# Kernel tuning notes

Measured on AMD Instinct MI355X. Metric: run time of the kernel, lower is better.

Reference implementation:

```python
import jax, jax.numpy as jnp
import numpy as np

N, E, T, D = 50000, 800000, 400000, 64


def _linear_params(key, fan_in, fan_out):
    kw, kb = jax.random.split(key)
    s = 1.0 / np.sqrt(fan_in)
    W = jax.random.uniform(kw, (fan_in, fan_out), minval=-s, maxval=s, dtype=jnp.float32)
    b = jax.random.uniform(kb, (fan_out,), minval=-s, maxval=s, dtype=jnp.float32)
    return W, b


def setup_inputs() -> dict:
    key = jax.random.key(0)
    ks = jax.random.split(key, 11)
    Ws1, bs1 = _linear_params(ks[0], 2 * D, D)
    Ws2, bs2 = _linear_params(ks[1], D, 3 * D)
    Wc1, bc1 = _linear_params(ks[2], 2 * D, D)
    Wc2, bc2 = _linear_params(ks[3], D, D)
    WV, bV = _linear_params(ks[4], D, D)
    return {
        "node_scalar": jax.random.normal(ks[5], (N, D), dtype=jnp.float32),
        "node_chiral": jax.random.normal(ks[6], (N, D), dtype=jnp.float32),
        "node_vector": jax.random.normal(ks[7], (N, 3, D), dtype=jnp.float32),
        "pos": jax.random.normal(ks[8], (N, 3), dtype=jnp.float32),
        "edge_index": jax.random.randint(ks[9], (E, 2), 0, N, dtype=jnp.int64),
        "triplet_index": jax.random.randint(ks[10], (T, 4), 0, N, dtype=jnp.int64),
        "Ws1": Ws1, "bs1": bs1, "Ws2": Ws2, "bs2": bs2,
        "Wc1": Wc1, "bc1": bc1, "Wc2": Wc2, "bc2": bc2,
        "WV": WV, "bV": bV,
    }


def reference(node_scalar, node_chiral, node_vector, pos, edge_index, triplet_index,
              Ws1, bs1, Ws2, bs2, Wc1, bc1, Wc2, bc2, WV, bV):
    n = node_scalar.shape[0]
    d = node_scalar.shape[1]
    e0, e1 = edge_index[:, 0], edge_index[:, 1]

    # Scalar / vector section: gather -> Linear-SiLU-Linear gate -> scatter-add
    g = jax.nn.silu(jnp.concatenate([node_scalar[e0], node_scalar[e1]], axis=1) @ Ws1 + bs1) @ Ws2 + bs2
    gate_vector, gate_edge, messages_ss = jnp.split(g, 3, axis=1)  # each [E, d]
    messages_vv = gate_vector[:, None, :] * node_vector[e1]               # [E, 3, d]
    rel = pos[e1] - pos[e0]                                               # [E, 3]
    messages_ev = gate_edge[:, None, :] * rel[:, :, None]                 # [E, 3, d]
    msg_ss = jax.ops.segment_sum(messages_ss, e0, num_segments=n)
    msg_vv = jax.ops.segment_sum(messages_vv, e0, num_segments=n)
    msg_ev = jax.ops.segment_sum(messages_ev, e0, num_segments=n)

    Vv = node_vector @ WV + bV          # [N, 3, d]
    Vv_norm = jnp.linalg.norm(Vv, axis=1)  # [N, d] (norm over spatial axis)
    message_vs = node_scalar * Vv_norm

    # Chiral section: triplet gathers, shared gate MLP, scalar triple product
    base, t1, t2, t3 = (triplet_index[:, i] for i in range(4))
    hc_base = node_chiral[base]

    def cgate(other):
        h = jnp.concatenate([hc_base, node_chiral[other]], axis=1)
        return jax.nn.silu(h @ Wc1 + bc1) @ Wc2 + bc2

    chiral_gate = cgate(t1) + cgate(t2) + cgate(t3)  # [T, d]
    pb = pos[base]
    r1, r2, r3 = pb - pos[t1], pb - pos[t2], pb - pos[t3]
    stp = jnp.einsum('ei,ei->e', r1, jnp.cross(r2, r3))  # scalar triple product [T]
    chiral_messages = chiral_gate / (stp + 0.01)[:, None]
    msg_chiral = jax.ops.segment_sum(chiral_messages, base, num_segments=n)

    return (node_scalar + msg_ss + message_vs,
            node_chiral + msg_chiral,
            node_vector + msg_vv + msg_ev)
```

## Files before the change

kernel.cpp:

```cpp
#include <hip/hip_runtime.h>
#include <math.h>

#define DD 64
typedef unsigned short ushort_t;
typedef __attribute__((ext_vector_type(8))) short bf16x8;
typedef __attribute__((ext_vector_type(4))) float f32x4;

__device__ __forceinline__ float silu_f(float x) {
    return x / (1.0f + __expf(-x));
}

__device__ __forceinline__ unsigned f32_to_bf16_rne(float x) {
    unsigned u = __float_as_uint(x);
    unsigned r = ((u >> 16) & 1u) + 0x7fffu;
    return (u + r) >> 16;
}

__device__ __forceinline__ float bf16_to_f32(ushort_t v) {
    return __uint_as_float(((unsigned)v) << 16);
}

__device__ __forceinline__ void gload_lds4(const void* gsrc, void* lds_base) {
    __builtin_amdgcn_global_load_lds(
        (const __attribute__((address_space(1))) void*)gsrc,
        (__attribute__((address_space(3))) void*)lds_base,
        4, 0, 0);
}

#define RFL(x) __builtin_amdgcn_readfirstlane(x)

__global__ __launch_bounds__(256) void rel_kernel(const int* __restrict__ eidx,
                                                  const float* __restrict__ pos,
                                                  float* __restrict__ relg, int E)
{
    int e = blockIdx.x * 256 + threadIdx.x;
    if (e < E) {
        int2 p = ((const int2*)eidx)[e];
        relg[3 * (size_t)e + 0] = pos[(size_t)p.y * 3 + 0] - pos[(size_t)p.x * 3 + 0];
        relg[3 * (size_t)e + 1] = pos[(size_t)p.y * 3 + 1] - pos[(size_t)p.x * 3 + 1];
        relg[3 * (size_t)e + 2] = pos[(size_t)p.y * 3 + 2] - pos[(size_t)p.x * 3 + 2];
    }
}

__global__ __launch_bounds__(256) void node_transform_kernel(
    const float* __restrict__ ns, const float* __restrict__ nc,
    const float* __restrict__ Ws1, const float* __restrict__ Wc1,
    ushort_t* __restrict__ Abf, ushort_t* __restrict__ Bbf,
    float* __restrict__ C, float* __restrict__ Dm,
    float* __restrict__ out1, int N)
{
    __shared__ float w1[128 * 64];
    __shared__ float wc1s[128 * 64];
    __shared__ float xs[4][2][64];
    __shared__ float ys[4][2][64];
    int tid = threadIdx.x;
    for (int i = tid; i < 128 * 64 / 4; i += 256) {
        ((float4*)w1)[i]   = ((const float4*)Ws1)[i];
        ((float4*)wc1s)[i] = ((const float4*)Wc1)[i];
    }
    __syncthreads();
    int wave = tid >> 6, lane = tid & 63;
    for (int nb = blockIdx.x * 8; nb < N; nb += gridDim.x * 8) {
        int n0 = nb + wave * 2;
        #pragma unroll
        for (int s = 0; s < 2; ++s) {
            int n = n0 + s;
            float xv = 0.f, yv = 0.f;
            if (n < N) { xv = ns[(size_t)n * DD + lane]; yv = nc[(size_t)n * DD + lane]; }
            xs[wave][s][lane] = xv;
            ys[wave][s][lane] = yv;
        }
        float aA[2] = {0.f, 0.f}, aB[2] = {0.f, 0.f}, aC[2] = {0.f, 0.f}, aD[2] = {0.f, 0.f};
        for (int k = 0; k < 64; ++k) {
            float wa  = w1[k * 64 + lane];
            float wb  = w1[(64 + k) * 64 + lane];
            float wca = wc1s[k * 64 + lane];
            float wcb = wc1s[(64 + k) * 64 + lane];
            #pragma unroll
            for (int s = 0; s < 2; ++s) {
                float xk = xs[wave][s][k];
                float yk = ys[wave][s][k];
                aA[s] += xk * wa;  aB[s] += xk * wb;
                aC[s] += yk * wca; aD[s] += yk * wcb;
            }
        }
        #pragma unroll
        for (int s = 0; s < 2; ++s) {
            int n = n0 + s;
            if (n < N) {
                Abf[(size_t)n * DD + lane] = (ushort_t)f32_to_bf16_rne(aA[s]);
                Bbf[(size_t)n * DD + lane] = (ushort_t)f32_to_bf16_rne(aB[s]);
                C[(size_t)n * DD + lane]  = aC[s];
                Dm[(size_t)n * DD + lane] = aD[s];
                out1[(size_t)n * DD + lane] = ys[wave][s][lane];
            }
        }
    }
}

__global__ __launch_bounds__(256) void node_vector_kernel(
    const float* __restrict__ ns, const float* __restrict__ nv,
    const float* __restrict__ WV, const float* __restrict__ bV,
    float* __restrict__ out0, float* __restrict__ out2,
    ushort_t* __restrict__ nvbf, int N)
{
    __shared__ float wv[64 * 64];
    __shared__ float vs[4][2][3][64];
    int tid = threadIdx.x;
    for (int i = tid; i < 64 * 64 / 4; i += 256)
        ((float4*)wv)[i] = ((const float4*)WV)[i];
    __syncthreads();
    int wave = tid >> 6, lane = tid & 63;
    float bVj = bV[lane];
    for (int nb = blockIdx.x * 8; nb < N; nb += gridDim.x * 8) {
        int n0 = nb + wave * 2;
        #pragma unroll
        for (int s = 0; s < 2; ++s) {
            int n = n0 + s;
            float v0 = 0.f, v1 = 0.f, v2 = 0.f;
            if (n < N) {
                v0 = nv[((size_t)n * 3 + 0) * DD + lane];
                v1 = nv[((size_t)n * 3 + 1) * DD + lane];
                v2 = nv[((size_t)n * 3 + 2) * DD + lane];
            }
            vs[wave][s][0][lane] = v0; vs[wave][s][1][lane] = v1; vs[wave][s][2][lane] = v2;
        }
        float a0[2], a1[2], a2[2];
        #pragma unroll
        for (int s = 0; s < 2; ++s) { a0[s] = bVj; a1[s] = bVj; a2[s] = bVj; }
        for (int k = 0; k < 64; ++k) {
            float w = wv[k * 64 + lane];
            #pragma unroll
            for (int s = 0; s < 2; ++s) {
                a0[s] += vs[wave][s][0][k] * w;
                a1[s] += vs[wave][s][1][k] * w;
                a2[s] += vs[wave][s][2][k] * w;
            }
        }
        #pragma unroll
        for (int s = 0; s < 2; ++s) {
            int n = n0 + s;
            if (n < N) {
                float norm = sqrtf(a0[s] * a0[s] + a1[s] * a1[s] + a2[s] * a2[s]);
                float x = ns[(size_t)n * DD + lane];
                out0[(size_t)n * DD + lane] = x * (1.f + norm);
                float v0 = vs[wave][s][0][lane], v1 = vs[wave][s][1][lane], v2 = vs[wave][s][2][lane];
                out2[((size_t)n * 3 + 0) * DD + lane] = v0;
                out2[((size_t)n * 3 + 1) * DD + lane] = v1;
                out2[((size_t)n * 3 + 2) * DD + lane] = v2;
                nvbf[((size_t)n * 3 + 0) * DD + lane] = (ushort_t)f32_to_bf16_rne(v0);
                nvbf[((size_t)n * 3 + 1) * DD + lane] = (ushort_t)f32_to_bf16_rne(v1);
                nvbf[((size_t)n * 3 + 2) * DD + lane] = (ushort_t)f32_to_bf16_rne(v2);
            }
        }
    }
}

#define GEPW 16
__global__ __launch_bounds__(256) void edge_kernel(
    const ushort_t* __restrict__ Abf, const ushort_t* __restrict__ Bbf,
    const ushort_t* __restrict__ nvbf, const float* __restrict__ relg,
    const int* __restrict__ eidx,
    const float* __restrict__ bs1, const float* __restrict__ Ws2, const float* __restrict__ bs2,
    float* __restrict__ out0, float* __restrict__ out2, int E)
{
    __shared__ unsigned w2frag[12 * 2 * 64 * 4];
    __shared__ ushort_t stAB[4][GEPW][128];
    __shared__ ushort_t stNV01[4][GEPW][132];
    __shared__ ushort_t stNV2[4][GEPW / 2][132];
    __shared__ float    relL[4][64];
    int tid = threadIdx.x;
    for (int i = tid; i < 12 * 2 * 64; i += 256) {
        int t  = i >> 7;
        int kk = (i >> 6) & 1;
        int l  = i & 63;
        int k0 = kk * 32 + (l >> 4) * 8;
        int col = t * 16 + (l & 15);
        #pragma unroll
        for (int jp = 0; jp < 4; ++jp) {
            float a = Ws2[(size_t)(k0 + 2 * jp) * 192 + col];
            float b = Ws2[(size_t)(k0 + 2 * jp + 1) * 192 + col];
            w2frag[i * 4 + jp] = f32_to_bf16_rne(a) | (f32_to_bf16_rne(b) << 16);
        }
    }
    __syncthreads();
    int wave = RFL(tid >> 6);
    int lane = tid & 63;
    float b1 = bs1[lane];
    float b2v_t[4], b2e_t[4], b2s_t[4];
    #pragma unroll
    for (int t = 0; t < 4; ++t) {
        b2v_t[t] = bs2[t * 16 + (lane & 15)];
        b2e_t[t] = bs2[64 + t * 16 + (lane & 15)];
        b2s_t[t] = bs2[128 + t * 16 + (lane & 15)];
    }

    long nG = ((long)E + GEPW - 1) / GEPW;
    for (long g = (long)blockIdx.x * 4 + wave; g < nG; g += (long)gridDim.x * 4) {
        long e0b = g * GEPW;
        int i0a[GEPW], i1a[GEPW];
        #pragma unroll
        for (int e = 0; e < GEPW; ++e) {
            long eid = e0b + e; if (eid >= E) eid = E - 1;
            int2 p = ((const int2*)eidx)[eid];
            i0a[e] = RFL(p.x); i1a[e] = RFL(p.y);
        }
        #pragma unroll
        for (int e = 0; e < GEPW; ++e) {
            const char* srcAB = (lane < 32)
                ? ((const char*)Abf + (size_t)i0a[e] * 128 + lane * 4)
                : ((const char*)Bbf + (size_t)i1a[e] * 128 + (lane - 32) * 4);
            gload_lds4(srcAB, &stAB[wave][e][0]);
            gload_lds4((const char*)nvbf + (size_t)i1a[e] * 384 + lane * 4, &stNV01[wave][e][0]);
        }
        #pragma unroll
        for (int p2 = 0; p2 < GEPW / 2; ++p2) {
            const char* src2 = (lane < 32)
                ? ((const char*)nvbf + (size_t)i1a[2 * p2] * 384 + 256 + lane * 4)
                : ((const char*)nvbf + (size_t)i1a[2 * p2 + 1] * 384 + 256 + (lane - 32) * 4);
            gload_lds4(src2, &stNV2[wave][p2][0]);
        }
        gload_lds4((const char*)relg + e0b * 12 + lane * 4, &relL[wave][0]);
        asm volatile("s_waitcnt vmcnt(0)" ::: "memory");
        __builtin_amdgcn_sched_barrier(0);
        #pragma unroll
        for (int e = 0; e < GEPW; ++e) {
            float a = bf16_to_f32(stAB[wave][e][lane]);
            float b = bf16_to_f32(stAB[wave][e][64 + lane]);
            float h = silu_f(a + b + b1);
            *(float*)((char*)&stAB[wave][e][0] + ((lane * 4) ^ ((e & 7) << 5))) = h;
        }
        __builtin_amdgcn_sched_barrier(0);
        f32x4 acc[12];
        f32x4 zz = {0.f, 0.f, 0.f, 0.f};
        #pragma unroll
        for (int t = 0; t < 12; ++t) acc[t] = zz;
        int row = lane & 15;
        #pragma unroll
        for (int kk = 0; kk < 2; ++kk) {
            int coff = (kk * 128 + ((lane >> 4) * 32)) ^ ((row & 7) << 5);
            const char* hp = (const char*)&stAB[wave][row][0] + coff;
            float4 lo = *(const float4*)hp;
            float4 hi = *(const float4*)(hp + 16);
            unsigned a0, a1, a2, a3;
            asm("v_cvt_pk_bf16_f32 %0, %1, %2" : "=v"(a0) : "v"(lo.x), "v"(lo.y));
            asm("v_cvt_pk_bf16_f32 %0, %1, %2" : "=v"(a1) : "v"(lo.z), "v"(lo.w));
            asm("v_cvt_pk_bf16_f32 %0, %1, %2" : "=v"(a2) : "v"(hi.x), "v"(hi.y));
            asm("v_cvt_pk_bf16_f32 %0, %1, %2" : "=v"(a3) : "v"(hi.z), "v"(hi.w));
            union { unsigned u[4]; bf16x8 v; } af;
            af.u[0] = a0; af.u[1] = a1; af.u[2] = a2; af.u[3] = a3;
            #pragma unroll
            for (int t = 0; t < 12; ++t) {
                bf16x8 bf = *(const bf16x8*)&w2frag[((t * 2 + kk) * 64 + lane) * 4];
                acc[t] = __builtin_amdgcn_mfma_f32_16x16x32_bf16(af.v, bf, acc[t], 0, 0, 0);
            }
        }
        int vi_all = 0;
        #pragma unroll
        for (int e = 0; e < GEPW; ++e) vi_all = (lane == e) ? i0a[e] : vi_all;
        int eLane0 = (lane >> 4) * 4;
        #pragma unroll
        for (int rg = 0; rg < 4; ++rg) {
            int e = eLane0 + rg;
            int i0 = __builtin_amdgcn_ds_bpermute(e * 4, vi_all);
            bool ok = (e0b + e) < E;
            float r0v = relL[wave][e * 3 + 0];
            float r1v = relL[wave][e * 3 + 1];
            float r2v = relL[wave][e * 3 + 2];
            #pragma unroll
            for (int t = 0; t < 4; ++t) {
                int dim = t * 16 + (lane & 15);
                float gv = acc[t][rg]     + b2v_t[t];
                float ge = acc[4 + t][rg] + b2e_t[t];
                float ss = acc[8 + t][rg] + b2s_t[t];
                float v0 = bf16_to_f32(stNV01[wave][e][dim]);
                float v1 = bf16_to_f32(stNV01[wave][e][64 + dim]);
                float v2 = bf16_to_f32(stNV2[wave][e >> 1][(e & 1) * 64 + dim]);
                if (ok) {
                    unsafeAtomicAdd(&out0[(size_t)(unsigned)i0 * 64u + dim], ss);
                    unsafeAtomicAdd(&out2[((size_t)(unsigned)i0 * 3u + 0) * 64u + dim], gv * v0 + ge * r0v);
                    unsafeAtomicAdd(&out2[((size_t)(unsigned)i0 * 3u + 1) * 64u + dim], gv * v1 + ge * r1v);
                    unsafeAtomicAdd(&out2[((size_t)(unsigned)i0 * 3u + 2) * 64u + dim], gv * v2 + ge * r2v);
                }
            }
        }
    }
}

#define TPW 4
__global__ __launch_bounds__(256) void triplet_kernel(
    const float* __restrict__ C, const float* __restrict__ Dm,
    const float* __restrict__ pos, const int* __restrict__ tidx,
    const float* __restrict__ bc1, const float* __restrict__ Wc2, const float* __restrict__ bc2,
    float* __restrict__ out1, int T)
{
    __shared__ float wT[64 * 64];
    __shared__ float stC[4][TPW][64];
    __shared__ float stD[4][TPW][3][64];
    int tid = threadIdx.x;
    for (int i = tid; i < 64 * 64 / 4; i += 256)
        ((float4*)wT)[i] = ((const float4*)Wc2)[i];
    __syncthreads();
    int wave = RFL(tid >> 6);
    int lane = tid & 63;
    float b1 = bc1[lane];
    float b2 = bc2[lane] * 3.0f;
    for (long bb = (long)blockIdx.x * (4 * TPW); bb < T; bb += (long)gridDim.x * (4 * TPW)) {
        long t0 = bb + wave * TPW;
        int ib[TPW], it1[TPW], it2[TPW], it3[TPW];
        #pragma unroll
        for (int e = 0; e < TPW; ++e) {
            long t = t0 + e;
            int b = 0, t1 = 0, t2 = 0, t3 = 0;
            if (t < T) { int4 q = ((const int4*)tidx)[t]; b = q.x; t1 = q.y; t2 = q.z; t3 = q.w; }
            ib[e]  = RFL(b);
            it1[e] = RFL(t1);
            it2[e] = RFL(t2);
            it3[e] = RFL(t3);
        }
        #pragma unroll
        for (int e = 0; e < TPW; ++e) {
            gload_lds4(C  + (size_t)ib[e]  * DD + lane, &stC[wave][e][0]);
            gload_lds4(Dm + (size_t)it1[e] * DD + lane, &stD[wave][e][0][0]);
            gload_lds4(Dm + (size_t)it2[e] * DD + lane, &stD[wave][e][1][0]);
            gload_lds4(Dm + (size_t)it3[e] * DD + lane, &stD[wave][e][2][0]);
        }
        asm volatile("s_waitcnt vmcnt(0)" ::: "memory");
        float inv[TPW];
        #pragma unroll
        for (int e = 0; e < TPW; ++e) {
            float hb = stC[wave][e][lane] + b1;
            float h = silu_f(hb + stD[wave][e][0][lane])
                    + silu_f(hb + stD[wave][e][1][lane])
                    + silu_f(hb + stD[wave][e][2][lane]);
            stC[wave][e][lane] = h;
            int b = ib[e], t1 = it1[e], t2 = it2[e], t3 = it3[e];
            double pbx = pos[(size_t)b * 3], pby = pos[(size_t)b * 3 + 1], pbz = pos[(size_t)b * 3 + 2];
            double r1x = pbx - pos[(size_t)t1 * 3], r1y = pby - pos[(size_t)t1 * 3 + 1], r1z = pbz - pos[(size_t)t1 * 3 + 2];
            double r2x = pbx - pos[(size_t)t2 * 3], r2y = pby - pos[(size_t)t2 * 3 + 1], r2z = pbz - pos[(size_t)t2 * 3 + 2];
            double r3x = pbx - pos[(size_t)t3 * 3], r3y = pby - pos[(size_t)t3 * 3 + 1], r3z = pbz - pos[(size_t)t3 * 3 + 2];
            double cx = r2y * r3z - r2z * r3y;
            double cy = r2z * r3x - r2x * r3z;
            double cz = r2x * r3y - r2y * r3x;
            double stp = r1x * cx + r1y * cy + r1z * cz;
            inv[e] = (float)(1.0 / (stp + 0.01));
        }
        float acc[TPW];
        #pragma unroll
        for (int e = 0; e < TPW; ++e) acc[e] = 0.f;
        for (int k4 = 0; k4 < 64; k4 += 4) {
            float4 hk[TPW];
            #pragma unroll
            for (int e = 0; e < TPW; ++e) hk[e] = *(const float4*)&stC[wave][e][k4];
            #pragma unroll
            for (int kk = 0; kk < 4; ++kk) {
                float wk = wT[(k4 + kk) * 64 + lane];
                #pragma unroll
                for (int e = 0; e < TPW; ++e) acc[e] += (&hk[e].x)[kk] * wk;
            }
        }
        #pragma unroll
        for (int e = 0; e < TPW; ++e) {
            long t = t0 + e;
            if (t >= T) break;
            unsafeAtomicAdd(&out1[(size_t)ib[e] * DD + lane], (acc[e] + b2) * inv[e]);
        }
    }
}

extern "C" void kernel_launch(void* const* d_in, const int* in_sizes, int n_in,
                              void* d_out, int out_size, void* d_ws, size_t ws_size,
                              hipStream_t stream)
{
    const float* ns  = (const float*)d_in[0];
    const float* nc  = (const float*)d_in[1];
    const float* nv  = (const float*)d_in[2];
    const float* pos = (const float*)d_in[3];
    const int* eidx  = (const int*)d_in[4];
    const int* tidx  = (const int*)d_in[5];
    const float* Ws1 = (const float*)d_in[6];
    const float* bs1 = (const float*)d_in[7];
    const float* Ws2 = (const float*)d_in[8];
    const float* bs2 = (const float*)d_in[9];
    const float* Wc1 = (const float*)d_in[10];
    const float* bc1 = (const float*)d_in[11];
    const float* Wc2 = (const float*)d_in[12];
    const float* bc2 = (const float*)d_in[13];
    const float* WV  = (const float*)d_in[14];
    const float* bV  = (const float*)d_in[15];

    int N = in_sizes[0] / 64;
    int E = in_sizes[4] / 2;
    int T = in_sizes[5] / 4;

    float* out0 = (float*)d_out;
    float* out1 = out0 + (size_t)N * 64;
    float* out2 = out1 + (size_t)N * 64;

    float* C    = (float*)d_ws;
    float* Dm   = C + (size_t)N * 64;
    float* relg = Dm + (size_t)N * 64;
    ushort_t* Abf  = (ushort_t*)(relg + (size_t)E * 3 + 64);
    ushort_t* Bbf  = Abf + (size_t)N * 64;
    ushort_t* nvbf = Bbf + (size_t)N * 64;

    rel_kernel<<<(E + 255) / 256, 256, 0, stream>>>(eidx, pos, relg, E);
    node_transform_kernel<<<2048, 256, 0, stream>>>(ns, nc, Ws1, Wc1, Abf, Bbf, C, Dm, out1, N);
    node_vector_kernel<<<2048, 256, 0, stream>>>(ns, nv, WV, bV, out0, out2, nvbf, N);
    edge_kernel<<<4096, 256, 0, stream>>>(Abf, Bbf, nvbf, relg, eidx, bs1, Ws2, bs2, out0, out2, E);
    triplet_kernel<<<4096, 256, 0, stream>>>(C, Dm, pos, tidx, bc1, Wc2, bc2, out1, T);
}
```

Baseline: 914.6 us.

## Sort edges by destination and aggregate per-lane before atomic scatter

Adds a counting sort of edges by destination node (histogram, single-block scan, atomic scatter) that also computes relative positions in sorted order. The edge kernel then reads the permuted edge list and accumulates contributions for consecutive edges with the same destination in registers, flushing with atomics only when the destination changes. This is meant to cut the number of global float atomics and their contention, at the cost of extra preprocessing launches and integer atomics.

Result: slower. 968.1 us (+5.9%).

```diff
diff --git a/kernel.cpp b/kernel.cpp
--- a/kernel.cpp
+++ b/kernel.cpp
@@ -29,16 +29,53 @@
 
 #define RFL(x) __builtin_amdgcn_readfirstlane(x)
 
-__global__ __launch_bounds__(256) void rel_kernel(const int* __restrict__ eidx,
-                                                  const float* __restrict__ pos,
-                                                  float* __restrict__ relg, int E)
-{
-    int e = blockIdx.x * 256 + threadIdx.x;
-    if (e < E) {
-        int2 p = ((const int2*)eidx)[e];
-        relg[3 * (size_t)e + 0] = pos[(size_t)p.y * 3 + 0] - pos[(size_t)p.x * 3 + 0];
-        relg[3 * (size_t)e + 1] = pos[(size_t)p.y * 3 + 1] - pos[(size_t)p.x * 3 + 1];
-        relg[3 * (size_t)e + 2] = pos[(size_t)p.y * 3 + 2] - pos[(size_t)p.x * 3 + 2];
+__global__ __launch_bounds__(256) void zero_kernel(int* p, int n) {
+    int i = blockIdx.x * 256 + threadIdx.x;
+    if (i < n) p[i] = 0;
+}
+
+__global__ __launch_bounds__(256) void hist_kernel(const int* __restrict__ eidx,
+                                                   int* __restrict__ counts, int E) {
+    int i = blockIdx.x * 256 + threadIdx.x;
+    if (i < E) atomicAdd(&counts[((const int2*)eidx)[i].x], 1);
+}
+
+__global__ __launch_bounds__(1024) void scan_kernel(const int* __restrict__ counts,
+                                                    int* __restrict__ cursor, int N) {
+    __shared__ int part[1024];
+    int tid = threadIdx.x;
+    int CH = (N + 1023) / 1024;
+    int lo = tid * CH, hi = lo + CH; if (hi > N) hi = N; if (lo > N) lo = N;
+    int s = 0;
+    for (int i = lo; i < hi; ++i) s += counts[i];
+    part[tid] = s;
+    __syncthreads();
+    for (int d = 1; d < 1024; d <<= 1) {
+        int v = (tid >= d) ? part[tid - d] : 0;
+        __syncthreads();
+        part[tid] += v;
+        __syncthreads();
+    }
+    int run = (tid == 0) ? 0 : part[tid - 1];
+    for (int i = lo; i < hi; ++i) {
+        cursor[i] = run;
+        run += counts[i];
+    }
+}
+
+__global__ __launch_bounds__(256) void scatter2_kernel(const int* __restrict__ eidx,
+                                                       const float* __restrict__ pos,
+                                                       int* __restrict__ cursor,
+                                                       int2* __restrict__ eperm,
+                                                       float* __restrict__ relg, int E) {
+    int i = blockIdx.x * 256 + threadIdx.x;
+    if (i < E) {
+        int2 p = ((const int2*)eidx)[i];
+        int dst = atomicAdd(&cursor[p.x], 1);
+        eperm[dst] = p;
+        relg[3 * (size_t)dst + 0] = pos[(size_t)p.y * 3 + 0] - pos[(size_t)p.x * 3 + 0];
+        relg[3 * (size_t)dst + 1] = pos[(size_t)p.y * 3 + 1] - pos[(size_t)p.x * 3 + 1];
+        relg[3 * (size_t)dst + 2] = pos[(size_t)p.y * 3 + 2] - pos[(size_t)p.x * 3 + 2];
     }
 }
 
@@ -160,7 +197,7 @@
 __global__ __launch_bounds__(256) void edge_kernel(
     const ushort_t* __restrict__ Abf, const ushort_t* __restrict__ Bbf,
     const ushort_t* __restrict__ nvbf, const float* __restrict__ relg,
-    const int* __restrict__ eidx,
+    const int2* __restrict__ eperm,
     const float* __restrict__ bs1, const float* __restrict__ Ws2, const float* __restrict__ bs2,
     float* __restrict__ out0, float* __restrict__ out2, int E)
 {
@@ -202,7 +239,7 @@
         #pragma unroll
         for (int e = 0; e < GEPW; ++e) {
             long eid = e0b + e; if (eid >= E) eid = E - 1;
-            int2 p = ((const int2*)eidx)[eid];
+            int2 p = eperm[eid];
             i0a[e] = RFL(p.x); i1a[e] = RFL(p.y);
         }
         #pragma unroll
@@ -259,30 +296,55 @@
         #pragma unroll
         for (int e = 0; e < GEPW; ++e) vi_all = (lane == e) ? i0a[e] : vi_all;
         int eLane0 = (lane >> 4) * 4;
+        float aS[4]  = {0.f, 0.f, 0.f, 0.f};
+        float aV0[4] = {0.f, 0.f, 0.f, 0.f};
+        float aV1[4] = {0.f, 0.f, 0.f, 0.f};
+        float aV2[4] = {0.f, 0.f, 0.f, 0.f};
+        int icur = __builtin_amdgcn_ds_bpermute(eLane0 * 4, vi_all);
         #pragma unroll
         for (int rg = 0; rg < 4; ++rg) {
             int e = eLane0 + rg;
             int i0 = __builtin_amdgcn_ds_bpermute(e * 4, vi_all);
             bool ok = (e0b + e) < E;
-            float r0v = relL[wave][e * 3 + 0];
-            float r1v = relL[wave][e * 3 + 1];
-            float r2v = relL[wave][e * 3 + 2];
-            #pragma unroll
-            for (int t = 0; t < 4; ++t) {
-                int dim = t * 16 + (lane & 15);
-                float gv = acc[t][rg]     + b2v_t[t];
-                float ge = acc[4 + t][rg] + b2e_t[t];
-                float ss = acc[8 + t][rg] + b2s_t[t];
-                float v0 = bf16_to_f32(stNV01[wave][e][dim]);
-                float v1 = bf16_to_f32(stNV01[wave][e][64 + dim]);
-                float v2 = bf16_to_f32(stNV2[wave][e >> 1][(e & 1) * 64 + dim]);
-                if (ok) {
-                    unsafeAtomicAdd(&out0[(size_t)(unsigned)i0 * 64u + dim], ss);
-                    unsafeAtomicAdd(&out2[((size_t)(unsigned)i0 * 3u + 0) * 64u + dim], gv * v0 + ge * r0v);
-                    unsafeAtomicAdd(&out2[((size_t)(unsigned)i0 * 3u + 1) * 64u + dim], gv * v1 + ge * r1v);
-                    unsafeAtomicAdd(&out2[((size_t)(unsigned)i0 * 3u + 2) * 64u + dim], gv * v2 + ge * r2v);
+            if (i0 != icur) {
+                #pragma unroll
+                for (int t = 0; t < 4; ++t) {
+                    int dim = t * 16 + (lane & 15);
+                    unsafeAtomicAdd(&out0[(size_t)(unsigned)icur * 64u + dim], aS[t]);
+                    unsafeAtomicAdd(&out2[((size_t)(unsigned)icur * 3u + 0) * 64u + dim], aV0[t]);
+                    unsafeAtomicAdd(&out2[((size_t)(unsigned)icur * 3u + 1) * 64u + dim], aV1[t]);
+                    unsafeAtomicAdd(&out2[((size_t)(unsigned)icur * 3u + 2) * 64u + dim], aV2[t]);
+                    aS[t] = 0.f; aV0[t] = 0.f; aV1[t] = 0.f; aV2[t] = 0.f;
                 }
-            }
+                icur = i0;
+            }
+            if (ok) {
+                float r0v = relL[wave][e * 3 + 0];
+                float r1v = relL[wave][e * 3 + 1];
+                float r2v = relL[wave][e * 3 + 2];
+                #pragma unroll
+                for (int t = 0; t < 4; ++t) {
+                    int dim = t * 16 + (lane & 15);
+                    float gv = acc[t][rg]     + b2v_t[t];
+                    float ge = acc[4 + t][rg] + b2e_t[t];
+                    float ss = acc[8 + t][rg] + b2s_t[t];
+                    float v0 = bf16_to_f32(stNV01[wave][e][dim]);
+                    float v1 = bf16_to_f32(stNV01[wave][e][64 + dim]);
+                    float v2 = bf16_to_f32(stNV2[wave][e >> 1][(e & 1) * 64 + dim]);
+                    aS[t]  += ss;
+                    aV0[t] += gv * v0 + ge * r0v;
+                    aV1[t] += gv * v1 + ge * r1v;
+                    aV2[t] += gv * v2 + ge * r2v;
+                }
+            }
+        }
+        #pragma unroll
+        for (int t = 0; t < 4; ++t) {
+            int dim = t * 16 + (lane & 15);
+            unsafeAtomicAdd(&out0[(size_t)(unsigned)icur * 64u + dim], aS[t]);
+            unsafeAtomicAdd(&out2[((size_t)(unsigned)icur * 3u + 0) * 64u + dim], aV0[t]);
+            unsafeAtomicAdd(&out2[((size_t)(unsigned)icur * 3u + 1) * 64u + dim], aV1[t]);
+            unsafeAtomicAdd(&out2[((size_t)(unsigned)icur * 3u + 2) * 64u + dim], aV2[t]);
         }
     }
 }
@@ -400,13 +462,19 @@
     float* C    = (float*)d_ws;
     float* Dm   = C + (size_t)N * 64;
     float* relg = Dm + (size_t)N * 64;
-    ushort_t* Abf  = (ushort_t*)(relg + (size_t)E * 3 + 64);
+    int2* eperm = (int2*)(relg + (size_t)E * 3 + 64);
+    int* counts = (int*)(eperm + (size_t)E);
+    int* cursor = counts + N;
+    ushort_t* Abf  = (ushort_t*)(cursor + N);
     ushort_t* Bbf  = Abf + (size_t)N * 64;
     ushort_t* nvbf = Bbf + (size_t)N * 64;
 
-    rel_kernel<<<(E + 255) / 256, 256, 0, stream>>>(eidx, pos, relg, E);
+    zero_kernel<<<(N + 255) / 256, 256, 0, stream>>>(counts, N);
+    hist_kernel<<<(E + 255) / 256, 256, 0, stream>>>(eidx, counts, E);
+    scan_kernel<<<1, 1024, 0, stream>>>(counts, cursor, N);
+    scatter2_kernel<<<(E + 255) / 256, 256, 0, stream>>>(eidx, pos, cursor, eperm, relg, E);
     node_transform_kernel<<<2048, 256, 0, stream>>>(ns, nc, Ws1, Wc1, Abf, Bbf, C, Dm, out1, N);
     node_vector_kernel<<<2048, 256, 0, stream>>>(ns, nv, WV, bV, out0, out2, nvbf, N);
-    edge_kernel<<<4096, 256, 0, stream>>>(Abf, Bbf, nvbf, relg, eidx, bs1, Ws2, bs2, out0, out2, E);
+    edge_kernel<<<4096, 256, 0, stream>>>(Abf, Bbf, nvbf, relg, eperm, bs1, Ws2, bs2, out0, out2, E);
     triplet_kernel<<<4096, 256, 0, stream>>>(C, Dm, pos, tidx, bc1, Wc2, bc2, out1, T);
 }
```

## Merge prep kernels into one launch and overlap edge gathers with MFMA

Applied to the files above, without the earlier changes.

Merges the relative-position, node-transform and node-vector kernels into one launch that dispatches on block index, so three short kernels no longer serialize. The fused kernel uses one 68 KB shared buffer sized for the largest branch, which can lower occupancy for the lighter branches. In the edge kernel, the node-vector gathers are issued after the A/B gathers, and a partial vmcnt wait lets the MFMA gate computation start while those loads are still in flight. A full wait is kept before the scatter phase. The partial-wait count is hand-tuned, so it would need updating if the load count per wave changes.

Result: no change. 925.7 us (+1.2%).

```diff
diff --git a/kernel.cpp b/kernel.cpp
--- a/kernel.cpp
+++ b/kernel.cpp
@@ -5,6 +5,9 @@
 typedef unsigned short ushort_t;
 typedef __attribute__((ext_vector_type(8))) short bf16x8;
 typedef __attribute__((ext_vector_type(4))) float f32x4;
+
+#define GEPW 16
+#define TPW 4
 
 __device__ __forceinline__ float silu_f(float x) {
     return x / (1.0f + __expf(-x));
@@ -29,134 +32,140 @@
 
 #define RFL(x) __builtin_amdgcn_readfirstlane(x)
 
-__global__ __launch_bounds__(256) void rel_kernel(const int* __restrict__ eidx,
-                                                  const float* __restrict__ pos,
-                                                  float* __restrict__ relg, int E)
-{
-    int e = blockIdx.x * 256 + threadIdx.x;
-    if (e < E) {
-        int2 p = ((const int2*)eidx)[e];
-        relg[3 * (size_t)e + 0] = pos[(size_t)p.y * 3 + 0] - pos[(size_t)p.x * 3 + 0];
-        relg[3 * (size_t)e + 1] = pos[(size_t)p.y * 3 + 1] - pos[(size_t)p.x * 3 + 1];
-        relg[3 * (size_t)e + 2] = pos[(size_t)p.y * 3 + 2] - pos[(size_t)p.x * 3 + 2];
-    }
-}
-
-__global__ __launch_bounds__(256) void node_transform_kernel(
+__global__ __launch_bounds__(256) void fused_prep_kernel(
+    const int* __restrict__ eidx, const float* __restrict__ pos, float* __restrict__ relg,
     const float* __restrict__ ns, const float* __restrict__ nc,
     const float* __restrict__ Ws1, const float* __restrict__ Wc1,
     ushort_t* __restrict__ Abf, ushort_t* __restrict__ Bbf,
-    float* __restrict__ C, float* __restrict__ Dm,
-    float* __restrict__ out1, int N)
+    float* __restrict__ C, float* __restrict__ Dm, float* __restrict__ out1,
+    const float* __restrict__ nv, const float* __restrict__ WV, const float* __restrict__ bV,
+    float* __restrict__ out0, float* __restrict__ out2, ushort_t* __restrict__ nvbf,
+    int N, int E, int relB)
 {
-    __shared__ float w1[128 * 64];
-    __shared__ float wc1s[128 * 64];
-    __shared__ float xs[4][2][64];
-    __shared__ float ys[4][2][64];
+    __shared__ __align__(16) char smem[69632];
     int tid = threadIdx.x;
-    for (int i = tid; i < 128 * 64 / 4; i += 256) {
-        ((float4*)w1)[i]   = ((const float4*)Ws1)[i];
-        ((float4*)wc1s)[i] = ((const float4*)Wc1)[i];
-    }
-    __syncthreads();
-    int wave = tid >> 6, lane = tid & 63;
-    for (int nb = blockIdx.x * 8; nb < N; nb += gridDim.x * 8) {
-        int n0 = nb + wave * 2;
-        #pragma unroll
-        for (int s = 0; s < 2; ++s) {
-            int n = n0 + s;
-            float xv = 0.f, yv = 0.f;
-            if (n < N) { xv = ns[(size_t)n * DD + lane]; yv = nc[(size_t)n * DD + lane]; }
-            xs[wave][s][lane] = xv;
-            ys[wave][s][lane] = yv;
-        }
-        float aA[2] = {0.f, 0.f}, aB[2] = {0.f, 0.f}, aC[2] = {0.f, 0.f}, aD[2] = {0.f, 0.f};
-        for (int k = 0; k < 64; ++k) {
-            float wa  = w1[k * 64 + lane];
-            float wb  = w1[(64 + k) * 64 + lane];
-            float wca = wc1s[k * 64 + lane];
-            float wcb = wc1s[(64 + k) * 64 + lane];
+    int bx = blockIdx.x;
+
+    if (bx < relB) {
+        int e = bx * 256 + tid;
+        if (e < E) {
+            int2 p = ((const int2*)eidx)[e];
+            relg[3 * (size_t)e + 0] = pos[(size_t)p.y * 3 + 0] - pos[(size_t)p.x * 3 + 0];
+            relg[3 * (size_t)e + 1] = pos[(size_t)p.y * 3 + 1] - pos[(size_t)p.x * 3 + 1];
+            relg[3 * (size_t)e + 2] = pos[(size_t)p.y * 3 + 2] - pos[(size_t)p.x * 3 + 2];
+        }
+        return;
+    }
+    if (bx < relB + 2048) {
+        int blk = bx - relB;
+        float* w1   = (float*)smem;
+        float* wc1s = (float*)(smem + 32768);
+        float* xs   = (float*)(smem + 65536);
+        float* ys   = (float*)(smem + 67584);
+        for (int i = tid; i < 128 * 64 / 4; i += 256) {
+            ((float4*)w1)[i]   = ((const float4*)Ws1)[i];
+            ((float4*)wc1s)[i] = ((const float4*)Wc1)[i];
+        }
+        __syncthreads();
+        int wave = tid >> 6, lane = tid & 63;
+        for (int nb = blk * 8; nb < N; nb += 2048 * 8) {
+            int n0 = nb + wave * 2;
             #pragma unroll
             for (int s = 0; s < 2; ++s) {
-                float xk = xs[wave][s][k];
-                float yk = ys[wave][s][k];
-                aA[s] += xk * wa;  aB[s] += xk * wb;
-                aC[s] += yk * wca; aD[s] += yk * wcb;
-            }
-        }
-        #pragma unroll
-        for (int s = 0; s < 2; ++s) {
-            int n = n0 + s;
-            if (n < N) {
-                Abf[(size_t)n * DD + lane] = (ushort_t)f32_to_bf16_rne(aA[s]);
-                Bbf[(size_t)n * DD + lane] = (ushort_t)f32_to_bf16_rne(aB[s]);
-                C[(size_t)n * DD + lane]  = aC[s];
-                Dm[(size_t)n * DD + lane] = aD[s];
-                out1[(size_t)n * DD + lane] = ys[wave][s][lane];
-            }
-        }
-    }
-}
-
-__global__ __launch_bounds__(256) void node_vector_kernel(
-    const float* __restrict__ ns, const float* __restrict__ nv,
-    const float* __restrict__ WV, const float* __restrict__ bV,
-    float* __restrict__ out0, float* __restrict__ out2,
-    ushort_t* __restrict__ nvbf, int N)
-{
-    __shared__ float wv[64 * 64];
-    __shared__ float vs[4][2][3][64];
-    int tid = threadIdx.x;
-    for (int i = tid; i < 64 * 64 / 4; i += 256)
-        ((float4*)wv)[i] = ((const float4*)WV)[i];
-    __syncthreads();
-    int wave = tid >> 6, lane = tid & 63;
-    float bVj = bV[lane];
-    for (int nb = blockIdx.x * 8; nb < N; nb += gridDim.x * 8) {
-        int n0 = nb + wave * 2;
-        #pragma unroll
-        for (int s = 0; s < 2; ++s) {
-            int n = n0 + s;
-            float v0 = 0.f, v1 = 0.f, v2 = 0.f;
-            if (n < N) {
-                v0 = nv[((size_t)n * 3 + 0) * DD + lane];
-                v1 = nv[((size_t)n * 3 + 1) * DD + lane];
-                v2 = nv[((size_t)n * 3 + 2) * DD + lane];
-            }
-            vs[wave][s][0][lane] = v0; vs[wave][s][1][lane] = v1; vs[wave][s][2][lane] = v2;
-        }
-        float a0[2], a1[2], a2[2];
-        #pragma unroll
-        for (int s = 0; s < 2; ++s) { a0[s] = bVj; a1[s] = bVj; a2[s] = bVj; }
-        for (int k = 0; k < 64; ++k) {
-            float w = wv[k * 64 + lane];
+                int n = n0 + s;
+                float xv = 0.f, yv = 0.f;
+                if (n < N) { xv = ns[(size_t)n * DD + lane]; yv = nc[(size_t)n * DD + lane]; }
+                xs[(wave * 2 + s) * 64 + lane] = xv;
+                ys[(wave * 2 + s) * 64 + lane] = yv;
+            }
+            float aA[2] = {0.f, 0.f}, aB[2] = {0.f, 0.f}, aC[2] = {0.f, 0.f}, aD[2] = {0.f, 0.f};
+            for (int k = 0; k < 64; ++k) {
+                float wa  = w1[k * 64 + lane];
+                float wb  = w1[(64 + k) * 64 + lane];
+                float wca = wc1s[k * 64 + lane];
+                float wcb = wc1s[(64 + k) * 64 + lane];
+                #pragma unroll
+                for (int s = 0; s < 2; ++s) {
+                    float xk = xs[(wave * 2 + s) * 64 + k];
+                    float yk = ys[(wave * 2 + s) * 64 + k];
+                    aA[s] += xk * wa;  aB[s] += xk * wb;
+                    aC[s] += yk * wca; aD[s] += yk * wcb;
+                }
+            }
             #pragma unroll
             for (int s = 0; s < 2; ++s) {
-                a0[s] += vs[wave][s][0][k] * w;
-                a1[s] += vs[wave][s][1][k] * w;
-                a2[s] += vs[wave][s][2][k] * w;
-            }
-        }
-        #pragma unroll
-        for (int s = 0; s < 2; ++s) {
-            int n = n0 + s;
-            if (n < N) {
-                float norm = sqrtf(a0[s] * a0[s] + a1[s] * a1[s] + a2[s] * a2[s]);
-                float x = ns[(size_t)n * DD + lane];
-                out0[(size_t)n * DD + lane] = x * (1.f + norm);
-                float v0 = vs[wave][s][0][lane], v1 = vs[wave][s][1][lane], v2 = vs[wave][s][2][lane];
-                out2[((size_t)n * 3 + 0) * DD + lane] = v0;
-                out2[((size_t)n * 3 + 1) * DD + lane] = v1;
-                out2[((size_t)n * 3 + 2) * DD + lane] = v2;
-                nvbf[((size_t)n * 3 + 0) * DD + lane] = (ushort_t)f32_to_bf16_rne(v0);
-                nvbf[((size_t)n * 3 + 1) * DD + lane] = (ushort_t)f32_to_bf16_rne(v1);
-                nvbf[((size_t)n * 3 + 2) * DD + lane] = (ushort_t)f32_to_bf16_rne(v2);
-            }
-        }
-    }
-}
-
-#define GEPW 16
+                int n = n0 + s;
+                if (n < N) {
+                    Abf[(size_t)n * DD + lane] = (ushort_t)f32_to_bf16_rne(aA[s]);
+                    Bbf[(size_t)n * DD + lane] = (ushort_t)f32_to_bf16_rne(aB[s]);
+                    C[(size_t)n * DD + lane]  = aC[s];
+                    Dm[(size_t)n * DD + lane] = aD[s];
+                    out1[(size_t)n * DD + lane] = ys[(wave * 2 + s) * 64 + lane];
+                }
+            }
+            __syncthreads();
+        }
+        return;
+    }
+    {
+        int blk = bx - relB - 2048;
+        float* wv = (float*)smem;
+        float* vs = (float*)(smem + 16384);
+        for (int i = tid; i < 64 * 64 / 4; i += 256)
+            ((float4*)wv)[i] = ((const float4*)WV)[i];
+        __syncthreads();
+        int wave = tid >> 6, lane = tid & 63;
+        float bVj = bV[lane];
+        for (int nb = blk * 8; nb < N; nb += 2048 * 8) {
+            int n0 = nb + wave * 2;
+            #pragma unroll
+            for (int s = 0; s < 2; ++s) {
+                int n = n0 + s;
+                float v0 = 0.f, v1 = 0.f, v2 = 0.f;
+                if (n < N) {
+                    v0 = nv[((size_t)n * 3 + 0) * DD + lane];
+                    v1 = nv[((size_t)n * 3 + 1) * DD + lane];
+                    v2 = nv[((size_t)n * 3 + 2) * DD + lane];
+                }
+                vs[((wave * 2 + s) * 3 + 0) * 64 + lane] = v0;
+                vs[((wave * 2 + s) * 3 + 1) * 64 + lane] = v1;
+                vs[((wave * 2 + s) * 3 + 2) * 64 + lane] = v2;
+            }
+            float a0[2], a1[2], a2[2];
+            #pragma unroll
+            for (int s = 0; s < 2; ++s) { a0[s] = bVj; a1[s] = bVj; a2[s] = bVj; }
+            for (int k = 0; k < 64; ++k) {
+                float w = wv[k * 64 + lane];
+                #pragma unroll
+                for (int s = 0; s < 2; ++s) {
+                    a0[s] += vs[((wave * 2 + s) * 3 + 0) * 64 + k] * w;
+                    a1[s] += vs[((wave * 2 + s) * 3 + 1) * 64 + k] * w;
+                    a2[s] += vs[((wave * 2 + s) * 3 + 2) * 64 + k] * w;
+                }
+            }
+            #pragma unroll
+            for (int s = 0; s < 2; ++s) {
+                int n = n0 + s;
+                if (n < N) {
+                    float norm = sqrtf(a0[s] * a0[s] + a1[s] * a1[s] + a2[s] * a2[s]);
+                    float x = ns[(size_t)n * DD + lane];
+                    out0[(size_t)n * DD + lane] = x * (1.f + norm);
+                    float v0 = vs[((wave * 2 + s) * 3 + 0) * 64 + lane];
+                    float v1 = vs[((wave * 2 + s) * 3 + 1) * 64 + lane];
+                    float v2 = vs[((wave * 2 + s) * 3 + 2) * 64 + lane];
+                    out2[((size_t)n * 3 + 0) * DD + lane] = v0;
+                    out2[((size_t)n * 3 + 1) * DD + lane] = v1;
+                    out2[((size_t)n * 3 + 2) * DD + lane] = v2;
+                    nvbf[((size_t)n * 3 + 0) * DD + lane] = (ushort_t)f32_to_bf16_rne(v0);
+                    nvbf[((size_t)n * 3 + 1) * DD + lane] = (ushort_t)f32_to_bf16_rne(v1);
+                    nvbf[((size_t)n * 3 + 2) * DD + lane] = (ushort_t)f32_to_bf16_rne(v2);
+                }
+            }
+            __syncthreads();
+        }
+    }
+}
+
 __global__ __launch_bounds__(256) void edge_kernel(
     const ushort_t* __restrict__ Abf, const ushort_t* __restrict__ Bbf,
     const ushort_t* __restrict__ nvbf, const float* __restrict__ relg,
@@ -164,11 +173,11 @@
     const float* __restrict__ bs1, const float* __restrict__ Ws2, const float* __restrict__ bs2,
     float* __restrict__ out0, float* __restrict__ out2, int E)
 {
-    __shared__ unsigned w2frag[12 * 2 * 64 * 4];
-    __shared__ ushort_t stAB[4][GEPW][128];
-    __shared__ ushort_t stNV01[4][GEPW][132];
-    __shared__ ushort_t stNV2[4][GEPW / 2][132];
-    __shared__ float    relL[4][64];
+    __shared__ __align__(16) unsigned w2frag[12 * 2 * 64 * 4];
+    __shared__ __align__(16) ushort_t stAB[4][GEPW][128];
+    __shared__ __align__(16) ushort_t stNV01[4][GEPW][132];
+    __shared__ __align__(16) ushort_t stNV2[4][GEPW / 2][132];
+    __shared__ __align__(16) float    relL[4][64];
     int tid = threadIdx.x;
     for (int i = tid; i < 12 * 2 * 64; i += 256) {
         int t  = i >> 7;
@@ -211,8 +220,11 @@
                 ? ((const char*)Abf + (size_t)i0a[e] * 128 + lane * 4)
                 : ((const char*)Bbf + (size_t)i1a[e] * 128 + (lane - 32) * 4);
             gload_lds4(srcAB, &stAB[wave][e][0]);
+        }
+        __builtin_amdgcn_sched_barrier(0);
+        #pragma unroll
+        for (int e = 0; e < GEPW; ++e)
             gload_lds4((const char*)nvbf + (size_t)i1a[e] * 384 + lane * 4, &stNV01[wave][e][0]);
-        }
         #pragma unroll
         for (int p2 = 0; p2 < GEPW / 2; ++p2) {
             const char* src2 = (lane < 32)
@@ -221,7 +233,8 @@
             gload_lds4(src2, &stNV2[wave][p2][0]);
         }
         gload_lds4((const char*)relg + e0b * 12 + lane * 4, &relL[wave][0]);
-        asm volatile("s_waitcnt vmcnt(0)" ::: "memory");
+        __builtin_amdgcn_sched_barrier(0);
+        asm volatile("s_waitcnt vmcnt(25)" ::: "memory");
         __builtin_amdgcn_sched_barrier(0);
         #pragma unroll
         for (int e = 0; e < GEPW; ++e) {
@@ -255,6 +268,8 @@
                 acc[t] = __builtin_amdgcn_mfma_f32_16x16x32_bf16(af.v, bf, acc[t], 0, 0, 0);
             }
         }
+        asm volatile("s_waitcnt vmcnt(0)" ::: "memory");
+        __builtin_amdgcn_sched_barrier(0);
         int vi_all = 0;
         #pragma unroll
         for (int e = 0; e < GEPW; ++e) vi_all = (lane == e) ? i0a[e] : vi_all;
@@ -287,7 +302,6 @@
     }
 }
 
-#define TPW 4
 __global__ __launch_bounds__(256) void triplet_kernel(
     const float* __restrict__ C, const float* __restrict__ Dm,
     const float* __restrict__ pos, const int* __restrict__ tidx,
@@ -404,9 +418,14 @@
     ushort_t* Bbf  = Abf + (size_t)N * 64;
     ushort_t* nvbf = Bbf + (size_t)N * 64;
 
-    rel_kernel<<<(E + 255) / 256, 256, 0, stream>>>(eidx, pos, relg, E);
-    node_transform_kernel<<<2048, 256, 0, stream>>>(ns, nc, Ws1, Wc1, Abf, Bbf, C, Dm, out1, N);
-    node_vector_kernel<<<2048, 256, 0, stream>>>(ns, nv, WV, bV, out0, out2, nvbf, N);
-    edge_kernel<<<4096, 256, 0, stream>>>(Abf, Bbf, nvbf, relg, eidx, bs1, Ws2, bs2, out0, out2, E);
+    int relB = (E + 255) / 256;
+
+    fused_prep_kernel<<<relB + 4096, 256, 0, stream>>>(
+        eidx, pos, relg,
+        ns, nc, Ws1, Wc1, Abf, Bbf, C, Dm, out1,
+        nv, WV, bV, out0, out2, nvbf,
+        N, E, relB);
+    edge_kernel<<<4096, 256, 0, stream>>>(Abf, Bbf, nvbf, relg, eidx,
+                                          bs1, Ws2, bs2, out0, out2, E);
     triplet_kernel<<<4096, 256, 0, stream>>>(C, Dm, pos, tidx, bc1, Wc2, bc2, out1, T);
 }
```
